# Optimization experiments

Measured on AMD Instinct MI355X. Metric: run time of the kernel, lower is better.

The kernel has to match this reference:

```python
import jax, jax.numpy as jnp
import numpy as np

V, E, H, DH, C, B, T = 50000, 256, 256, 512, 5, 64, 2048


def setup_inputs() -> dict:
    key = jax.random.key(0)
    ks = jax.random.split(key, 10)
    s = lambda k, sh: (jax.random.normal(k, sh, jnp.float32) * 0.05)
    seqs = jax.random.randint(ks[0], (B, T), 0, V)
    # descending sorted lengths, max length == T (matches max_len = sorted_lens[0])
    lens = jnp.sort(jax.random.randint(ks[1], (B,), T // 4, T + 1))[::-1]
    lens = lens.at[0].set(T).astype(jnp.int32)
    return {
        "seqs": seqs, "lens": lens,
        "emb": s(ks[2], (V, E)),
        "W_ih_f": s(ks[3], (3 * H, E)), "W_hh_f": s(ks[4], (3 * H, H)),
        "b_ih_f": jnp.zeros(3 * H, jnp.float32), "b_hh_f": jnp.zeros(3 * H, jnp.float32),
        "W_ih_b": s(ks[5], (3 * H, E)), "W_hh_b": s(ks[6], (3 * H, H)),
        "b_ih_b": jnp.zeros(3 * H, jnp.float32), "b_hh_b": jnp.zeros(3 * H, jnp.float32),
        "W1": s(ks[7], (DH, 2 * H)), "b1": jnp.zeros(DH, jnp.float32),
        "W2": s(ks[8], (C, DH)), "b2": jnp.zeros(C, jnp.float32),
    }


def _gru_scan(xs, W_ih, W_hh, b_ih, b_hh):
    """xs: [T,B,E]; torch GRUCell semantics, gate order r,z,n. Returns final h [B,H]."""
    gi = jnp.einsum('tbe,ge->tbg', xs, W_ih) + b_ih  # input projections, all steps

    def step(h, gi_t):
        gh = h @ W_hh.T + b_hh
        ir, iz, i_n = jnp.split(gi_t, 3, axis=-1)
        hr, hz, hn = jnp.split(gh, 3, axis=-1)
        r = jax.nn.sigmoid(ir + hr)
        z = jax.nn.sigmoid(iz + hz)
        n = jnp.tanh(i_n + r * hn)
        return (1.0 - z) * n + z * h, None

    h0 = jnp.zeros((xs.shape[1], W_hh.shape[1]), xs.dtype)
    hT, _ = jax.lax.scan(step, h0, gi)
    return hT


def reference(seqs, lens, emb, W_ih_f, W_hh_f, b_ih_f, b_hh_f,
              W_ih_b, W_hh_b, b_ih_b, b_hh_b, W1, b1, W2, b2):
    x = emb[seqs]  # [B,T,E]
    # original LEFT-pads embedded sequences with zeros to max_len
    valid = (jnp.arange(T)[None, :] >= (T - lens)[:, None]).astype(x.dtype)  # [B,T]
    x = x * valid[:, :, None]
    xs = jnp.swapaxes(x, 0, 1)  # [T,B,E]
    hf = _gru_scan(xs, W_ih_f, W_hh_f, b_ih_f, b_hh_f)
    hb = _gru_scan(xs[::-1], W_ih_b, W_hh_b, b_ih_b, b_hh_b)
    rep = jnp.concatenate([hf, hb], axis=1)  # [B,2H]
    h1 = jax.nn.relu(rep @ W1.T + b1)  # dropout is identity in eval
    return jax.nn.softmax(h1 @ W2.T + b2, axis=-1)
```

## Files before the change

### kernel.cpp

```cpp
#include <hip/hip_runtime.h>
#include <stdint.h>

typedef uint32_t u32; typedef uint16_t u16;
typedef __attribute__((ext_vector_type(8))) __bf16 bf16x8;
typedef __attribute__((ext_vector_type(4))) float f32x4;
typedef __attribute__((ext_vector_type(2))) u32 u32x2;
typedef __attribute__((ext_vector_type(4))) u32 u32x4;

#define Vv 50000
#define Ee 256
#define Hh 256
#define Gg 768
#define Bb 64
#define Tt 2048

__device__ __forceinline__ u16 f2bf(float f) {
  u32 x = __builtin_bit_cast(u32, f);
  return (u16)((x + 0x7FFFu + ((x >> 16) & 1u)) >> 16);
}
__device__ __forceinline__ float bf2f(u16 b) {
  u32 x = ((u32)b) << 16;
  return __builtin_bit_cast(float, x);
}
__device__ __forceinline__ u32 pack2(float a, float b) {
  return (u32)f2bf(a) | ((u32)f2bf(b) << 16);
}
__device__ __forceinline__ float sigm(float x) {
  float e = __builtin_amdgcn_exp2f(-1.44269504089f * x);
  return __builtin_amdgcn_rcpf(1.0f + e);
}
__device__ __forceinline__ float tanh_fast(float x) {
  float e = __builtin_amdgcn_exp2f(2.88539008178f * x);
  return 1.0f - 2.0f * __builtin_amdgcn_rcpf(e + 1.0f);
}
__device__ __forceinline__ float bfx(u32x2 v, int q) {
  u32 word = (q & 2) ? v[1] : v[0];
  u16 h = (q & 1) ? (u16)(word >> 16) : (u16)(word & 0xffffu);
  return bf2f(h);
}

__global__ void k0_bias(const float* __restrict__ bih_f, const float* __restrict__ bhh_f,
                        const float* __restrict__ bih_b, const float* __restrict__ bhh_b,
                        u16* __restrict__ Pf, u16* __restrict__ Pb) {
  int c = threadIdx.x + blockIdx.x * 256;
  if (c < Gg) {
    float bf_ = bih_f[c] + (c < 512 ? bhh_f[c] : 0.f);
    float bb_ = bih_b[c] + (c < 512 ? bhh_b[c] : 0.f);
    Pf[(size_t)Vv * Gg + c] = f2bf(bf_);
    Pb[(size_t)Vv * Gg + c] = f2bf(bb_);
  }
}

__global__ __launch_bounds__(256) void k1_proj(
    const float* __restrict__ emb, const float* __restrict__ Wih_f,
    const float* __restrict__ Wih_b,
    const float* __restrict__ bih_f, const float* __restrict__ bhh_f,
    const float* __restrict__ bih_b, const float* __restrict__ bhh_b,
    u16* __restrict__ Pf, u16* __restrict__ Pb)
{
  const int t = threadIdx.x, w = t >> 6, l = t & 63;
  const int cl = l & 15, rq = l >> 4;
  const int m0 = blockIdx.x * 128;
  const int n0 = blockIdx.y * 64;
  const int dir = blockIdx.z;
  const float* Wih = dir ? Wih_b : Wih_f;
  const float* bih = dir ? bih_b : bih_f;
  const float* bhh = dir ? bhh_b : bhh_f;
  u16* Pd = dir ? Pb : Pf;

  __shared__ __align__(16) u16 As[128 * 40];
  __shared__ __align__(16) u16 Bs[64 * 40];

  f32x4 zero4 = {0.f, 0.f, 0.f, 0.f};
  f32x4 acc[4][2];
#pragma unroll
  for (int i = 0; i < 4; ++i)
#pragma unroll
    for (int j = 0; j < 2; ++j) acc[i][j] = zero4;

  const int mw = (w >> 1) * 64;
  const int nw = (w & 1) * 32;

  for (int kt = 0; kt < 8; ++kt) {
#pragma unroll
    for (int j = 0; j < 4; ++j) {
      const int flat = t * 4 + j * 1024;
      const int row = flat >> 5, col = flat & 31;
      const int gm = m0 + row;
      float4 v = {0.f, 0.f, 0.f, 0.f};
      if (gm < Vv) v = *(const float4*)(emb + (size_t)gm * Ee + kt * 32 + col);
      u32* d = (u32*)(As + row * 40 + col);
      d[0] = pack2(v.x, v.y);
      d[1] = pack2(v.z, v.w);
    }
#pragma unroll
    for (int j = 0; j < 2; ++j) {
      const int flat = t * 4 + j * 1024;
      const int row = flat >> 5, col = flat & 31;
      const float4 v = *(const float4*)(Wih + (size_t)(n0 + row) * Ee + kt * 32 + col);
      u32* d = (u32*)(Bs + row * 40 + col);
      d[0] = pack2(v.x, v.y);
      d[1] = pack2(v.z, v.w);
    }
    __syncthreads();
    bf16x8 a[4], bfr[2];
#pragma unroll
    for (int mt = 0; mt < 4; ++mt)
      a[mt] = *(const bf16x8*)(As + (mw + mt * 16 + cl) * 40 + rq * 8);
#pragma unroll
    for (int nt = 0; nt < 2; ++nt)
      bfr[nt] = *(const bf16x8*)(Bs + (nw + nt * 16 + cl) * 40 + rq * 8);
#pragma unroll
    for (int mt = 0; mt < 4; ++mt)
#pragma unroll
      for (int nt = 0; nt < 2; ++nt)
        acc[mt][nt] = __builtin_amdgcn_mfma_f32_16x16x32_bf16(a[mt], bfr[nt], acc[mt][nt], 0, 0, 0);
    __syncthreads();
  }
#pragma unroll
  for (int mt = 0; mt < 4; ++mt)
#pragma unroll
    for (int nt = 0; nt < 2; ++nt)
#pragma unroll
      for (int q = 0; q < 4; ++q) {
        const int row = m0 + mw + mt * 16 + rq * 4 + q;
        const int col = n0 + nw + nt * 16 + cl;
        if (row < Vv) {
          const float bias = bih[col] + (col < 512 ? bhh[col] : 0.f);
          Pd[(size_t)row * Gg + col] = f2bf(acc[mt][nt][q] + bias);
        }
      }
}

__global__ __launch_bounds__(512, 1) __attribute__((amdgpu_waves_per_eu(2)))
void k2_rec(
    const int* __restrict__ seqs, const int* __restrict__ lens,
    const float* __restrict__ Whh_f, const float* __restrict__ Whh_b,
    const float* __restrict__ bhh_f, const float* __restrict__ bhh_b,
    const u16* __restrict__ Pf, const u16* __restrict__ Pb,
    float* __restrict__ rep)
{
  const int tid = threadIdx.x;
  const int w = tid >> 6, l = tid & 63;
  const int cl = l & 15, rq = l >> 4;
  const int dir = (int)blockIdx.x >> 2;
  const int b0 = ((int)blockIdx.x & 3) * 16;

  const float* Whh = dir ? Whh_b : Whh_f;
  const float* bhh = dir ? bhh_b : bhh_f;
  const u16* P = dir ? Pb : Pf;

  __shared__ __align__(16) u16 h_lds[2 * 16 * 264];

  bf16x8 wfrag[3][2][8];
#pragma unroll
  for (int g = 0; g < 3; ++g)
#pragma unroll
    for (int bi = 0; bi < 2; ++bi) {
      const int c = g * 256 + (2 * w + bi) * 16 + cl;
      const float* wr = Whh + (size_t)c * Hh;
#pragma unroll
      for (int kb = 0; kb < 8; ++kb) {
        const int k0 = kb * 32 + rq * 8;
        const float4 f0 = *(const float4*)(wr + k0);
        const float4 f1 = *(const float4*)(wr + k0 + 4);
        u32x4 uv = { pack2(f0.x, f0.y), pack2(f0.z, f0.w),
                     pack2(f1.x, f1.y), pack2(f1.z, f1.w) };
        wfrag[g][bi][kb] = __builtin_bit_cast(bf16x8, uv);
      }
    }

  float bhhn[2][4];
#pragma unroll
  for (int bi = 0; bi < 2; ++bi)
#pragma unroll
    for (int q = 0; q < 4; ++q)
      bhhn[bi][q] = bhh[512 + (2 * w + bi) * 16 + rq * 4 + q];

  float hprev[2][4];
#pragma unroll
  for (int bi = 0; bi < 2; ++bi)
#pragma unroll
    for (int q = 0; q < 4; ++q) hprev[bi][q] = 0.f;

  const int myrow = b0 + cl;
  const int mylen = lens[myrow];
  const int* myseq = seqs + (size_t)myrow * Tt;

  for (int i = tid; i < 16 * 264; i += 512) h_lds[i] = 0;

  u32x2 gi[3][2];
  {
    const int tok0 = myseq[dir ? (Tt - 1) : 0];
    const int valid0 = dir ? (0 < mylen) : (0 >= Tt - mylen);
    const size_t vrow = valid0 ? (size_t)tok0 : (size_t)Vv;
#pragma unroll
    for (int bi = 0; bi < 2; ++bi) {
      const u16* pr = P + vrow * Gg + (2 * w + bi) * 16 + rq * 4;
#pragma unroll
      for (int g = 0; g < 3; ++g) gi[g][bi] = *(const u32x2*)(pr + g * 256);
    }
  }
  __syncthreads();

  const int rdbase = cl * 264 + rq * 8;
  const int wrbase = cl * 264 + 2 * w * 16 + rq * 4;

  for (int s = 0; s < Tt; ++s) {
    const int par = s & 1;
    const u16* hb = h_lds + par * (16 * 264);
    u16* hn = h_lds + (par ^ 1) * (16 * 264);

    int tok1 = 0;
    const bool more = (s + 1 < Tt);
    if (more) tok1 = myseq[dir ? (Tt - 2 - s) : (s + 1)];

    f32x4 acc[3][2];
    f32x4 z4 = {0.f, 0.f, 0.f, 0.f};
#pragma unroll
    for (int g = 0; g < 3; ++g)
#pragma unroll
      for (int bi = 0; bi < 2; ++bi) acc[g][bi] = z4;

    bf16x8 bA = *(const bf16x8*)(hb + rdbase);
    bf16x8 bB;
#pragma unroll
    for (int kb = 0; kb < 8; kb += 2) {
      bB = *(const bf16x8*)(hb + rdbase + (kb + 1) * 32);
#pragma unroll
      for (int g = 0; g < 3; ++g)
#pragma unroll
        for (int bi = 0; bi < 2; ++bi)
          acc[g][bi] = __builtin_amdgcn_mfma_f32_16x16x32_bf16(wfrag[g][bi][kb], bA, acc[g][bi], 0, 0, 0);
      if (kb + 2 < 8) bA = *(const bf16x8*)(hb + rdbase + (kb + 2) * 32);
#pragma unroll
      for (int g = 0; g < 3; ++g)
#pragma unroll
        for (int bi = 0; bi < 2; ++bi)
          acc[g][bi] = __builtin_amdgcn_mfma_f32_16x16x32_bf16(wfrag[g][bi][kb + 1], bB, acc[g][bi], 0, 0, 0);
    }

#pragma unroll
    for (int bi = 0; bi < 2; ++bi) {
      float hq[4];
#pragma unroll
      for (int q = 0; q < 4; ++q) {
        const float ir = bfx(gi[0][bi], q);
        const float iz = bfx(gi[1][bi], q);
        const float in_ = bfx(gi[2][bi], q);
        const float r = sigm(ir + acc[0][bi][q]);
        const float z = sigm(iz + acc[1][bi][q]);
        const float n = tanh_fast(in_ + r * (acc[2][bi][q] + bhhn[bi][q]));
        const float hv = n + z * (hprev[bi][q] - n);
        hprev[bi][q] = hv;
        hq[q] = hv;
      }
      u32x2 hw = { pack2(hq[0], hq[1]), pack2(hq[2], hq[3]) };
      *(u32x2*)(hn + wrbase + bi * 16) = hw;

      if (more) {
        const int sn = s + 1;
        const int valid1 = dir ? (sn < mylen) : (sn >= Tt - mylen);
        const size_t vrow = valid1 ? (size_t)tok1 : (size_t)Vv;
        const u16* pr = P + vrow * Gg + (2 * w + bi) * 16 + rq * 4;
#pragma unroll
        for (int g = 0; g < 3; ++g) gi[g][bi] = *(const u32x2*)(pr + g * 256);
      }
    }

    __syncthreads();
  }

#pragma unroll
  for (int bi = 0; bi < 2; ++bi)
#pragma unroll
    for (int q = 0; q < 4; ++q) {
      const int col = (2 * w + bi) * 16 + rq * 4 + q;
      rep[(size_t)(b0 + cl) * (2 * Hh) + dir * Hh + col] = hprev[bi][q];
    }
}

__global__ __launch_bounds__(256) void k3a(
    const float* __restrict__ rep, const float* __restrict__ W1,
    const float* __restrict__ b1, float* __restrict__ h1)
{
  __shared__ float rl[512];
  const int b = blockIdx.x, t = threadIdx.x;
  rl[t] = rep[(size_t)b * 512 + t];
  rl[t + 256] = rep[(size_t)b * 512 + 256 + t];
  __syncthreads();
#pragma unroll
  for (int oo = 0; oo < 2; ++oo) {
    const int o = t + oo * 256;
    const float4* wr = (const float4*)(W1 + (size_t)o * 512);
    const float4* rr = (const float4*)rl;
    float acc = 0.f;
#pragma unroll 8
    for (int k = 0; k < 128; ++k) {
      const float4 wv = wr[k], rv = rr[k];
      acc += wv.x * rv.x + wv.y * rv.y + wv.z * rv.z + wv.w * rv.w;
    }
    h1[(size_t)b * 512 + o] = fmaxf(acc + b1[o], 0.f);
  }
}

__global__ __launch_bounds__(320) void k3b(
    const float* __restrict__ h1, const float* __restrict__ W2,
    const float* __restrict__ b2, float* __restrict__ out)
{
  __shared__ float lg[64 * 5];
  const int t = threadIdx.x;
  const int c = t >> 6, b = t & 63;
  const float4* hr = (const float4*)(h1 + (size_t)b * 512);
  const float4* wr = (const float4*)(W2 + (size_t)c * 512);
  float acc = 0.f;
#pragma unroll 8
  for (int k = 0; k < 128; ++k) {
    const float4 hv = hr[k], wv = wr[k];
    acc += hv.x * wv.x + hv.y * wv.y + hv.z * wv.z + hv.w * wv.w;
  }
  lg[b * 5 + c] = acc + b2[c];
  __syncthreads();
  if (t < 64) {
    float v[5];
#pragma unroll
    for (int i = 0; i < 5; ++i) v[i] = lg[t * 5 + i];
    float m = v[0];
#pragma unroll
    for (int i = 1; i < 5; ++i) m = fmaxf(m, v[i]);
    float ssum = 0.f;
#pragma unroll
    for (int i = 0; i < 5; ++i) {
      v[i] = __builtin_amdgcn_exp2f(1.44269504089f * (v[i] - m));
      ssum += v[i];
    }
    const float inv = 1.0f / ssum;
#pragma unroll
    for (int i = 0; i < 5; ++i) out[t * 5 + i] = v[i] * inv;
  }
}

extern "C" void kernel_launch(void* const* d_in, const int* in_sizes, int n_in,
                              void* d_out, int out_size, void* d_ws, size_t ws_size,
                              hipStream_t stream) {
  const int* seqs = (const int*)d_in[0];
  const int* lens = (const int*)d_in[1];
  const float* emb = (const float*)d_in[2];
  const float* Wih_f = (const float*)d_in[3];
  const float* Whh_f = (const float*)d_in[4];
  const float* bih_f = (const float*)d_in[5];
  const float* bhh_f = (const float*)d_in[6];
  const float* Wih_b = (const float*)d_in[7];
  const float* Whh_b = (const float*)d_in[8];
  const float* bih_b = (const float*)d_in[9];
  const float* bhh_b = (const float*)d_in[10];
  const float* W1 = (const float*)d_in[11];
  const float* b1 = (const float*)d_in[12];
  const float* W2 = (const float*)d_in[13];
  const float* b2 = (const float*)d_in[14];
  float* out = (float*)d_out;

  char* ws = (char*)d_ws;
  const size_t PSZ = (size_t)(Vv + 1) * Gg * 2;
  u16* Pf = (u16*)ws;
  u16* Pb = (u16*)(ws + PSZ);
  float* rep = (float*)(ws + 2 * PSZ);
  float* h1 = (float*)(ws + 2 * PSZ + 131072);

  hipLaunchKernelGGL(k0_bias, dim3(3), dim3(256), 0, stream,
                     bih_f, bhh_f, bih_b, bhh_b, Pf, Pb);
  hipLaunchKernelGGL(k1_proj, dim3(391, 12, 2), dim3(256), 0, stream,
                     emb, Wih_f, Wih_b, bih_f, bhh_f, bih_b, bhh_b, Pf, Pb);
  hipLaunchKernelGGL(k2_rec, dim3(8), dim3(512), 0, stream,
                     seqs, lens, Whh_f, Whh_b, bhh_f, bhh_b, Pf, Pb, rep);
  hipLaunchKernelGGL(k3a, dim3(64), dim3(256), 0, stream, rep, W1, b1, h1);
  hipLaunchKernelGGL(k3b, dim3(1), dim3(320), 0, stream, h1, W2, b2, out);
}
```

Baseline: 5.103 ms.

## Restructure projection GEMM tiling and streamline GRU recurrence step with swizzled LDS

The projection kernel now loads a 128-row embedding tile into LDS once and loops over all 12 output column blocks, instead of reloading it for each of 12 grid blocks. The recurrent kernel switches to a swizzled LDS layout for h with no padding, and starts the n-gate accumulator from the bias. It also prefetches tokens two steps ahead, uses a hardware bf16 pack instruction, and replaces __syncthreads with a lighter lgkmcnt wait plus barrier. These changes target the serial per-step latency of the 2048-step recurrence and the redundant embedding reads and conversions. In exchange, the projection grid has far fewer blocks, so less parallelism is available for that GEMM.

```diff
diff --git a/kernel.cpp b/kernel.cpp
--- a/kernel.cpp
+++ b/kernel.cpp
@@ -37,6 +37,11 @@
   u32 word = (q & 2) ? v[1] : v[0];
   u16 h = (q & 1) ? (u16)(word >> 16) : (u16)(word & 0xffffu);
   return bf2f(h);
+}
+__device__ __forceinline__ void block_sync_lds() {
+  asm volatile("s_waitcnt lgkmcnt(0)" ::: "memory");
+  __builtin_amdgcn_s_barrier();
+  asm volatile("" ::: "memory");
 }
 
 __global__ void k0_bias(const float* __restrict__ bih_f, const float* __restrict__ bhh_f,
@@ -61,87 +66,90 @@
   const int t = threadIdx.x, w = t >> 6, l = t & 63;
   const int cl = l & 15, rq = l >> 4;
   const int m0 = blockIdx.x * 128;
-  const int n0 = blockIdx.y * 64;
-  const int dir = blockIdx.z;
+  const int dir = blockIdx.y;
   const float* Wih = dir ? Wih_b : Wih_f;
   const float* bih = dir ? bih_b : bih_f;
   const float* bhh = dir ? bhh_b : bhh_f;
   u16* Pd = dir ? Pb : Pf;
 
-  __shared__ __align__(16) u16 As[128 * 40];
-  __shared__ __align__(16) u16 Bs[64 * 40];
-
-  f32x4 zero4 = {0.f, 0.f, 0.f, 0.f};
-  f32x4 acc[4][2];
-#pragma unroll
-  for (int i = 0; i < 4; ++i)
-#pragma unroll
-    for (int j = 0; j < 2; ++j) acc[i][j] = zero4;
-
-  const int mw = (w >> 1) * 64;
-  const int nw = (w & 1) * 32;
-
-  for (int kt = 0; kt < 8; ++kt) {
-#pragma unroll
-    for (int j = 0; j < 4; ++j) {
-      const int flat = t * 4 + j * 1024;
-      const int row = flat >> 5, col = flat & 31;
-      const int gm = m0 + row;
-      float4 v = {0.f, 0.f, 0.f, 0.f};
-      if (gm < Vv) v = *(const float4*)(emb + (size_t)gm * Ee + kt * 32 + col);
-      u32* d = (u32*)(As + row * 40 + col);
-      d[0] = pack2(v.x, v.y);
-      d[1] = pack2(v.z, v.w);
-    }
-#pragma unroll
-    for (int j = 0; j < 2; ++j) {
-      const int flat = t * 4 + j * 1024;
-      const int row = flat >> 5, col = flat & 31;
-      const float4 v = *(const float4*)(Wih + (size_t)(n0 + row) * Ee + kt * 32 + col);
-      u32* d = (u32*)(Bs + row * 40 + col);
-      d[0] = pack2(v.x, v.y);
-      d[1] = pack2(v.z, v.w);
+  __shared__ __align__(16) u16 As[4096 * 8];
+  __shared__ __align__(16) u16 Bs[2048 * 8];
+
+  for (int i = t; i < 4096; i += 256) {
+    const int kt = i >> 9, rem = i & 511, row = rem >> 2, rqv = rem & 3;
+    const int gm = m0 + row;
+    float4 a0 = {0.f,0.f,0.f,0.f}, a1 = {0.f,0.f,0.f,0.f};
+    if (gm < Vv) {
+      const float* src = emb + (size_t)gm * Ee + kt * 32 + rqv * 8;
+      a0 = *(const float4*)src;
+      a1 = *(const float4*)(src + 4);
+    }
+    u32x4 uv = { pack2(a0.x, a0.y), pack2(a0.z, a0.w),
+                 pack2(a1.x, a1.y), pack2(a1.z, a1.w) };
+    *(u32x4*)(As + (size_t)i * 8) = uv;
+  }
+  __syncthreads();
+
+  for (int nb = 0; nb < 12; ++nb) {
+    for (int i = t; i < 2048; i += 256) {
+      const int kt = i >> 8, rem = i & 255, r2 = rem >> 2, rqv = rem & 3;
+      const float* src = Wih + (size_t)(nb * 64 + r2) * Ee + kt * 32 + rqv * 8;
+      const float4 b0 = *(const float4*)src;
+      const float4 b1 = *(const float4*)(src + 4);
+      u32x4 uv = { pack2(b0.x, b0.y), pack2(b0.z, b0.w),
+                   pack2(b1.x, b1.y), pack2(b1.z, b1.w) };
+      *(u32x4*)(Bs + (size_t)i * 8) = uv;
     }
     __syncthreads();
-    bf16x8 a[4], bfr[2];
-#pragma unroll
-    for (int mt = 0; mt < 4; ++mt)
-      a[mt] = *(const bf16x8*)(As + (mw + mt * 16 + cl) * 40 + rq * 8);
-#pragma unroll
-    for (int nt = 0; nt < 2; ++nt)
-      bfr[nt] = *(const bf16x8*)(Bs + (nw + nt * 16 + cl) * 40 + rq * 8);
-#pragma unroll
-    for (int mt = 0; mt < 4; ++mt)
-#pragma unroll
-      for (int nt = 0; nt < 2; ++nt)
-        acc[mt][nt] = __builtin_amdgcn_mfma_f32_16x16x32_bf16(a[mt], bfr[nt], acc[mt][nt], 0, 0, 0);
-    __syncthreads();
-  }
-#pragma unroll
-  for (int mt = 0; mt < 4; ++mt)
-#pragma unroll
-    for (int nt = 0; nt < 2; ++nt)
-#pragma unroll
-      for (int q = 0; q < 4; ++q) {
-        const int row = m0 + mw + mt * 16 + rq * 4 + q;
-        const int col = n0 + nw + nt * 16 + cl;
-        if (row < Vv) {
-          const float bias = bih[col] + (col < 512 ? bhh[col] : 0.f);
-          Pd[(size_t)row * Gg + col] = f2bf(acc[mt][nt][q] + bias);
+
+    f32x4 zero4 = {0.f, 0.f, 0.f, 0.f};
+    f32x4 acc[2][4];
+#pragma unroll
+    for (int mt = 0; mt < 2; ++mt)
+#pragma unroll
+      for (int nt = 0; nt < 4; ++nt) acc[mt][nt] = zero4;
+
+#pragma unroll
+    for (int kt = 0; kt < 8; ++kt) {
+      bf16x8 af[2], bfr[4];
+#pragma unroll
+      for (int mt = 0; mt < 2; ++mt)
+        af[mt] = *(const bf16x8*)(As + ((size_t)kt * 512 + (w * 32 + mt * 16 + cl) * 4 + rq) * 8);
+#pragma unroll
+      for (int nt = 0; nt < 4; ++nt)
+        bfr[nt] = *(const bf16x8*)(Bs + ((size_t)kt * 256 + (nt * 16 + cl) * 4 + rq) * 8);
+#pragma unroll
+      for (int mt = 0; mt < 2; ++mt)
+#pragma unroll
+        for (int nt = 0; nt < 4; ++nt)
+          acc[mt][nt] = __builtin_amdgcn_mfma_f32_16x16x32_bf16(af[mt], bfr[nt], acc[mt][nt], 0, 0, 0);
+    }
+
+#pragma unroll
+    for (int mt = 0; mt < 2; ++mt)
+#pragma unroll
+      for (int nt = 0; nt < 4; ++nt) {
+        const int col = nb * 64 + nt * 16 + cl;
+        float bias = bih[col];
+        if (col < 512) bias += bhh[col];
+#pragma unroll
+        for (int q = 0; q < 4; ++q) {
+          const int row = m0 + w * 32 + mt * 16 + rq * 4 + q;
+          if (row < Vv) Pd[(size_t)row * Gg + col] = f2bf(acc[mt][nt][q] + bias);
         }
       }
-}
-
-__global__ __launch_bounds__(512, 1) __attribute__((amdgpu_waves_per_eu(2)))
-void k2_rec(
+    __syncthreads();
+  }
+}
+
+__global__ __launch_bounds__(512, 2) void k2_rec(
     const int* __restrict__ seqs, const int* __restrict__ lens,
     const float* __restrict__ Whh_f, const float* __restrict__ Whh_b,
     const float* __restrict__ bhh_f, const float* __restrict__ bhh_b,
     const u16* __restrict__ Pf, const u16* __restrict__ Pb,
     float* __restrict__ rep)
 {
-  const int tid = threadIdx.x;
-  const int w = tid >> 6, l = tid & 63;
+  const int tid = threadIdx.x, w = tid >> 6, l = tid & 63;
   const int cl = l & 15, rq = l >> 4;
   const int dir = (int)blockIdx.x >> 2;
   const int b0 = ((int)blockIdx.x & 3) * 16;
@@ -150,7 +158,7 @@
   const float* bhh = dir ? bhh_b : bhh_f;
   const u16* P = dir ? Pb : Pf;
 
-  __shared__ __align__(16) u16 h_lds[2 * 16 * 264];
+  __shared__ __align__(16) u16 h_lds[8192];
 
   bf16x8 wfrag[3][2][8];
 #pragma unroll
@@ -170,12 +178,8 @@
       }
     }
 
-  float bhhn[2][4];
-#pragma unroll
-  for (int bi = 0; bi < 2; ++bi)
-#pragma unroll
-    for (int q = 0; q < 4; ++q)
-      bhhn[bi][q] = bhh[512 + (2 * w + bi) * 16 + rq * 4 + q];
+  const float* bhhn0 = bhh + 512 + w * 32 + rq * 4;
+  const float* bhhn1 = bhhn0 + 16;
 
   float hprev[2][4];
 #pragma unroll
@@ -186,96 +190,99 @@
   const int myrow = b0 + cl;
   const int mylen = lens[myrow];
   const int* myseq = seqs + (size_t)myrow * Tt;
-
-  for (int i = tid; i < 16 * 264; i += 512) h_lds[i] = 0;
-
-  u32x2 gi[3][2];
+  const int vthr = Tt - mylen;
+
+  for (int i = tid; i < 4096; i += 512) ((u32*)h_lds)[i] = 0;
+
+  const int xk = (cl >> 1);
+  const int rdoff = cl * 64 + (((rq + xk) & 3) << 4);
+  const int wr0 = w * 1024 + cl * 64 + ((((rq >> 1) + xk) & 3) << 4) + (rq & 1) * 8;
+  const int wr1 = w * 1024 + cl * 64 + ((((rq >> 1) + 2 + xk) & 3) << 4) + (rq & 1) * 8;
+
+  const int colb0 = w * 32 + rq * 4;
+
+  u32x2 gi0[3], gi1[3];
   {
-    const int tok0 = myseq[dir ? (Tt - 1) : 0];
-    const int valid0 = dir ? (0 < mylen) : (0 >= Tt - mylen);
-    const size_t vrow = valid0 ? (size_t)tok0 : (size_t)Vv;
-#pragma unroll
-    for (int bi = 0; bi < 2; ++bi) {
-      const u16* pr = P + vrow * Gg + (2 * w + bi) * 16 + rq * 4;
-#pragma unroll
-      for (int g = 0; g < 3; ++g) gi[g][bi] = *(const u32x2*)(pr + g * 256);
-    }
-  }
-  __syncthreads();
-
-  const int rdbase = cl * 264 + rq * 8;
-  const int wrbase = cl * 264 + 2 * w * 16 + rq * 4;
-
+    const int tk = myseq[dir ? (Tt - 1) : 0];
+    const int valid = dir ? (0 < mylen) : (0 >= vthr);
+    const u32 off = (valid ? (u32)tk : (u32)Vv) * (u32)(Gg * 2);
+    const u16* pr = (const u16*)((const char*)P + off) + colb0;
+#pragma unroll
+    for (int g = 0; g < 3; ++g) {
+      gi0[g] = *(const u32x2*)(pr + g * 256);
+      gi1[g] = *(const u32x2*)(pr + g * 256 + 16);
+    }
+  }
+  int tok1 = myseq[dir ? (Tt - 2) : 1];
+  block_sync_lds();
+
+  int bb = 0;
+#pragma unroll 1
   for (int s = 0; s < Tt; ++s) {
-    const int par = s & 1;
-    const u16* hb = h_lds + par * (16 * 264);
-    u16* hn = h_lds + (par ^ 1) * (16 * 264);
-
-    int tok1 = 0;
-    const bool more = (s + 1 < Tt);
-    if (more) tok1 = myseq[dir ? (Tt - 2 - s) : (s + 1)];
-
-    f32x4 acc[3][2];
-    f32x4 z4 = {0.f, 0.f, 0.f, 0.f};
-#pragma unroll
-    for (int g = 0; g < 3; ++g)
-#pragma unroll
-      for (int bi = 0; bi < 2; ++bi) acc[g][bi] = z4;
-
-    bf16x8 bA = *(const bf16x8*)(hb + rdbase);
-    bf16x8 bB;
-#pragma unroll
-    for (int kb = 0; kb < 8; kb += 2) {
-      bB = *(const bf16x8*)(hb + rdbase + (kb + 1) * 32);
-#pragma unroll
-      for (int g = 0; g < 3; ++g)
-#pragma unroll
-        for (int bi = 0; bi < 2; ++bi)
-          acc[g][bi] = __builtin_amdgcn_mfma_f32_16x16x32_bf16(wfrag[g][bi][kb], bA, acc[g][bi], 0, 0, 0);
-      if (kb + 2 < 8) bA = *(const bf16x8*)(hb + rdbase + (kb + 2) * 32);
-#pragma unroll
-      for (int g = 0; g < 3; ++g)
-#pragma unroll
-        for (int bi = 0; bi < 2; ++bi)
-          acc[g][bi] = __builtin_amdgcn_mfma_f32_16x16x32_bf16(wfrag[g][bi][kb + 1], bB, acc[g][bi], 0, 0, 0);
-    }
-
-#pragma unroll
-    for (int bi = 0; bi < 2; ++bi) {
-      float hq[4];
-#pragma unroll
-      for (int q = 0; q < 4; ++q) {
-        const float ir = bfx(gi[0][bi], q);
-        const float iz = bfx(gi[1][bi], q);
-        const float in_ = bfx(gi[2][bi], q);
-        const float r = sigm(ir + acc[0][bi][q]);
-        const float z = sigm(iz + acc[1][bi][q]);
-        const float n = tanh_fast(in_ + r * (acc[2][bi][q] + bhhn[bi][q]));
-        const float hv = n + z * (hprev[bi][q] - n);
-        hprev[bi][q] = hv;
-        hq[q] = hv;
-      }
-      u32x2 hw = { pack2(hq[0], hq[1]), pack2(hq[2], hq[3]) };
-      *(u32x2*)(hn + wrbase + bi * 16) = hw;
-
-      if (more) {
-        const int sn = s + 1;
-        const int valid1 = dir ? (sn < mylen) : (sn >= Tt - mylen);
-        const size_t vrow = valid1 ? (size_t)tok1 : (size_t)Vv;
-        const u16* pr = P + vrow * Gg + (2 * w + bi) * 16 + rq * 4;
-#pragma unroll
-        for (int g = 0; g < 3; ++g) gi[g][bi] = *(const u32x2*)(pr + g * 256);
-      }
-    }
-
-    __syncthreads();
+    const char* hb = (const char*)h_lds + bb;
+    char* hn = (char*)h_lds + (bb ^ 8192);
+
+    f32x4 zero4 = {0.f, 0.f, 0.f, 0.f};
+    f32x4 ar0 = zero4, az0 = zero4, ar1 = zero4, az1 = zero4;
+    f32x4 an0 = *(const f32x4*)bhhn0;
+    f32x4 an1 = *(const f32x4*)bhhn1;
+
+#pragma unroll
+    for (int kb = 0; kb < 8; ++kb) {
+      const bf16x8 hf = *(const bf16x8*)(hb + kb * 1024 + rdoff);
+      ar0 = __builtin_amdgcn_mfma_f32_16x16x32_bf16(wfrag[0][0][kb], hf, ar0, 0, 0, 0);
+      az0 = __builtin_amdgcn_mfma_f32_16x16x32_bf16(wfrag[1][0][kb], hf, az0, 0, 0, 0);
+      an0 = __builtin_amdgcn_mfma_f32_16x16x32_bf16(wfrag[2][0][kb], hf, an0, 0, 0, 0);
+      ar1 = __builtin_amdgcn_mfma_f32_16x16x32_bf16(wfrag[0][1][kb], hf, ar1, 0, 0, 0);
+      az1 = __builtin_amdgcn_mfma_f32_16x16x32_bf16(wfrag[1][1][kb], hf, az1, 0, 0, 0);
+      an1 = __builtin_amdgcn_mfma_f32_16x16x32_bf16(wfrag[2][1][kb], hf, an1, 0, 0, 0);
+    }
+
+    int tok2 = tok1;
+    if (s + 2 < Tt) tok2 = myseq[dir ? (Tt - 3 - s) : (s + 2)];
+
+    const int validn = dir ? (s + 1 < mylen) : (s + 1 >= vthr);
+    const u32 offn = (validn ? (u32)tok1 : (u32)Vv) * (u32)(Gg * 2);
+    const u16* prn = (const u16*)((const char*)P + offn) + colb0;
+
+#define GATES(BI, GIS, AR, AZ, AN, WRO, PRADD)                                   \
+    {                                                                            \
+      float hq[4];                                                               \
+      _Pragma("unroll")                                                          \
+      for (int q = 0; q < 4; ++q) {                                              \
+        const float ir = bfx(GIS[0], q);                                         \
+        const float iz = bfx(GIS[1], q);                                         \
+        const float in_ = bfx(GIS[2], q);                                        \
+        const float r = sigm(ir + AR[q]);                                        \
+        const float z = sigm(iz + AZ[q]);                                        \
+        const float n = tanh_fast(fmaf(r, AN[q], in_));                          \
+        const float hv = fmaf(z, hprev[BI][q] - n, n);                           \
+        hprev[BI][q] = hv;                                                       \
+        hq[q] = hv;                                                              \
+      }                                                                          \
+      u32 p0, p1;                                                                \
+      asm("v_cvt_pk_bf16_f32 %0, %1, %2" : "=v"(p0) : "v"(hq[0]), "v"(hq[1]));   \
+      asm("v_cvt_pk_bf16_f32 %0, %1, %2" : "=v"(p1) : "v"(hq[2]), "v"(hq[3]));   \
+      u32x2 hw = {p0, p1};                                                       \
+      *(u32x2*)(hn + (bb ^ 8192) * 0 + WRO) = hw;                                \
+      _Pragma("unroll")                                                          \
+      for (int g = 0; g < 3; ++g) GIS[g] = *(const u32x2*)(prn + g * 256 + PRADD); \
+    }
+
+    GATES(0, gi0, ar0, az0, an0, wr0, 0)
+    GATES(1, gi1, ar1, az1, an1, wr1, 16)
+#undef GATES
+
+    tok1 = tok2;
+    bb ^= 8192;
+    block_sync_lds();
   }
 
 #pragma unroll
   for (int bi = 0; bi < 2; ++bi)
 #pragma unroll
     for (int q = 0; q < 4; ++q) {
-      const int col = (2 * w + bi) * 16 + rq * 4 + q;
+      const int col = w * 32 + bi * 16 + rq * 4 + q;
       rep[(size_t)(b0 + cl) * (2 * Hh) + dir * Hh + col] = hprev[bi][q];
     }
 }
@@ -369,7 +376,7 @@
 
   hipLaunchKernelGGL(k0_bias, dim3(3), dim3(256), 0, stream,
                      bih_f, bhh_f, bih_b, bhh_b, Pf, Pb);
-  hipLaunchKernelGGL(k1_proj, dim3(391, 12, 2), dim3(256), 0, stream,
+  hipLaunchKernelGGL(k1_proj, dim3(391, 2), dim3(256), 0, stream,
                      emb, Wih_f, Wih_b, bih_f, bhh_f, bih_b, bhh_b, Pf, Pb);
   hipLaunchKernelGGL(k2_rec, dim3(8), dim3(512), 0, stream,
                      seqs, lens, Whh_f, Whh_b, bhh_f, bhh_b, Pf, Pb, rep);
```

After: 6.093 ms. +19.4%, slower.
